# Optimization experiments

Hardware: AMD Instinct MI355X
Metric: run time of the kernel (lower is better)

The kernel has to match this reference:

```python
import jax, jax.numpy as jnp
import numpy as np

EMBED_DIM = 768
HEAD_SIZE = 64

def setup_inputs() -> dict:
    key = jax.random.key(0)
    k1, k2, k3, k4 = jax.random.split(key, 4)
    x = jax.random.normal(k1, (4, 4096, EMBED_DIM), dtype=jnp.float32)
    # nn.Linear(E, H, bias=False) weights, stored as [E, H] for y = x @ W
    scale = 1.0 / np.sqrt(EMBED_DIM)
    Wk = jax.random.uniform(k2, (EMBED_DIM, HEAD_SIZE), jnp.float32, -scale, scale)
    Wq = jax.random.uniform(k3, (EMBED_DIM, HEAD_SIZE), jnp.float32, -scale, scale)
    Wv = jax.random.uniform(k4, (EMBED_DIM, HEAD_SIZE), jnp.float32, -scale, scale)
    return {"x": x, "Wk": Wk, "Wq": Wq, "Wv": Wv}

def reference(x, Wk, Wq, Wv):
    # x: [B, S, E]
    E = x.shape[2]
    K = jnp.einsum("bse,eh->bsh", x, Wk)  # [B, S, H]
    Q = jnp.einsum("bse,eh->bsh", x, Wq)
    V = jnp.einsum("bse,eh->bsh", x, Wv)
    # NOTE: original scales by embedding_dim**0.5, not head_size**0.5
    A = jnp.einsum("bqh,bkh->bqk", Q, K) / jnp.sqrt(jnp.asarray(E, x.dtype))
    A = jax.nn.softmax(A, axis=-1)
    # dropout is inference-mode identity
    return jnp.einsum("bqk,bkh->bqh", A, V)
```

## Files before the change

### kernel.cpp

```cpp
#include <hip/hip_runtime.h>

typedef __attribute__((ext_vector_type(8))) short short8;
typedef __attribute__((ext_vector_type(4))) short short4v;
typedef __attribute__((ext_vector_type(4))) float float4v;

__device__ __forceinline__ short f2bf(float f) {
    union { float f; unsigned u; } v; v.f = f;
    return (short)((v.u + 0x7fffu + ((v.u >> 16) & 1u)) >> 16);
}

__device__ __forceinline__ float fast_exp2(float x) {
#if __has_builtin(__builtin_amdgcn_exp2f)
    return __builtin_amdgcn_exp2f(x);
#else
    return exp2f(x);
#endif
}

__device__ __forceinline__ unsigned cvt_pk_bf16(float lo, float hi) {
    unsigned r;
    asm("v_cvt_pk_bf16_f32 %0, %1, %2" : "=v"(r) : "v"(lo), "v"(hi));
    return r;
}

__global__ void wtrans_kernel(const float* __restrict__ Wk, const float* __restrict__ Wq,
                              const float* __restrict__ Wv, short* __restrict__ Wt3T) {
    int idx = blockIdx.x * 256 + threadIdx.x;
    int p = idx / 12288;
    int rem = idx - p * 12288;
    int kstep = rem / 512;
    int r2 = rem - kstep * 512;
    int lane = r2 >> 3, i = r2 & 7;
    int quad = lane >> 4, l16 = lane & 15;
    int j = p >> 2, nt = p & 3;
    int n = nt * 16 + l16;
    int k = kstep * 32 + quad * 8 + i;
    const float* W = (j == 0) ? Wq : (j == 1 ? Wk : Wv);
    float scale = (j == 0) ? 0.05205877f : 1.0f;
    Wt3T[idx] = f2bf(W[k * 64 + n] * scale);
}

__global__ __launch_bounds__(256, 4) void proj_kernel(
    const float* __restrict__ x, const short* __restrict__ Wt3T,
    short* __restrict__ Qs, short* __restrict__ Kb, short* __restrict__ Vtr)
{
    __shared__ alignas(16) int Abuf[3][256];
    __shared__ alignas(16) short sm[16 * 72];
    const int tid = threadIdx.x;
    const int wave = tid >> 6, lane = tid & 63, quad = lane >> 4, l16 = lane & 15;
    const int m0 = blockIdx.x * 16;
    const int p0 = wave * 3;

    const int xrow = tid >> 4, xcol = (tid & 15) * 2;
    const float* xp = x + (size_t)(m0 + xrow) * 768 + xcol;
    const int aidx = xrow * 16 + (tid & 15);
    const short* wt0 = Wt3T + (size_t)(p0 * 24) * 512 + lane * 8;

    float4v acc[3];
#pragma unroll
    for (int t = 0; t < 3; ++t) acc[t] = (float4v){0.f, 0.f, 0.f, 0.f};

    {
        float2 u = *(const float2*)xp;
        Abuf[0][aidx] = ((unsigned short)f2bf(u.x)) | ((unsigned)f2bf(u.y) << 16);
    }
    short8 Wc0 = *(const short8*)(wt0);
    short8 Wc1 = *(const short8*)(wt0 + 12288);
    short8 Wc2 = *(const short8*)(wt0 + 24576);
    float2 Xn = *(const float2*)(xp + 32);
    __syncthreads();

#pragma unroll
    for (int it = 0; it < 24; ++it) {
        short8 Wn0, Wn1, Wn2;
        float2 Xn2;
        if (it < 23) {
            const short* wn = wt0 + (it + 1) * 512;
            Wn0 = *(const short8*)(wn);
            Wn1 = *(const short8*)(wn + 12288);
            Wn2 = *(const short8*)(wn + 24576);
        }
        if (it < 22) Xn2 = *(const float2*)(xp + (it + 2) * 32);

        short8 a = *(const short8*)((const short*)Abuf[it % 3] + l16 * 32 + quad * 8);
        acc[0] = __builtin_amdgcn_mfma_f32_16x16x32_bf16(a, Wc0, acc[0], 0, 0, 0);
        acc[1] = __builtin_amdgcn_mfma_f32_16x16x32_bf16(a, Wc1, acc[1], 0, 0, 0);
        acc[2] = __builtin_amdgcn_mfma_f32_16x16x32_bf16(a, Wc2, acc[2], 0, 0, 0);

        if (it < 23)
            Abuf[(it + 1) % 3][aidx] = ((unsigned short)f2bf(Xn.x)) | ((unsigned)f2bf(Xn.y) << 16);
        Xn = Xn2;
        Wc0 = Wn0; Wc1 = Wn1; Wc2 = Wn2;
        __syncthreads();
    }

#pragma unroll
    for (int t = 0; t < 3; ++t) {
        const int p = p0 + t, j = p >> 2, nt = p & 3;
        if (j < 2) {
            short* dst = (j == 0) ? Qs : Kb;
#pragma unroll
            for (int r = 0; r < 4; ++r)
                dst[(size_t)(m0 + quad * 4 + r) * 64 + nt * 16 + l16] = f2bf(acc[t][r]);
        } else {
#pragma unroll
            for (int r = 0; r < 4; ++r)
                sm[(quad * 4 + r) * 72 + nt * 16 + l16] = f2bf(acc[t][r]);
        }
    }
    __syncthreads();
    {
        const int h = tid >> 2, si = (tid & 3) * 4;
        const int b = m0 >> 12, s0 = m0 & 4095;
        const int sb = s0 + si;
        const int jb = (sb & ~63) | (sb & 0x23) | ((sb & 0x0C) << 1) | ((sb & 0x10) >> 2);
        short4v tmp;
#pragma unroll
        for (int i = 0; i < 4; ++i) tmp[i] = sm[(si + i) * 72 + h];
        *(short4v*)(Vtr + (size_t)(b * 64 + h) * 4096 + jb) = tmp;
    }
}

__global__ __launch_bounds__(256, 2) void attn_kernel(
    const short* __restrict__ Qs, const short* __restrict__ Kb, const short* __restrict__ Vt,
    float* __restrict__ Opart, float* __restrict__ Ll, int kv_len)
{
    __shared__ alignas(16) short Kl[64 * 72];
    __shared__ alignas(16) short Vl[64 * 72];

    const int tid = threadIdx.x;
    const int wave = tid >> 6, lane = tid & 63, quad = lane >> 4, l16 = lane & 15;
    const int qt = blockIdx.x, b = blockIdx.y, sp = blockIdx.z;
    const int q0 = qt * 128;
    const int bS = b * 4096;
    const int kv0 = sp * kv_len;

    short8 qb[2][2];
#pragma unroll
    for (int ntq = 0; ntq < 2; ++ntq)
#pragma unroll
        for (int ks = 0; ks < 2; ++ks)
            qb[ntq][ks] = *(const short8*)(Qs + (size_t)(bS + q0 + wave * 32 + ntq * 16 + l16) * 64 + ks * 32 + quad * 8);

    float4v o[2][4];
#pragma unroll
    for (int ntq = 0; ntq < 2; ++ntq)
#pragma unroll
        for (int nt = 0; nt < 4; ++nt) o[ntq][nt] = (float4v){0.f, 0.f, 0.f, 0.f};
    float rs[2] = {0.f, 0.f};

    const int sr = tid >> 2, sc = (tid & 3) * 16;

    const short* ksrc0 = Kb + (size_t)(bS + kv0 + sr) * 64 + sc;
    const short* vsrc0 = Vt + (size_t)(b * 64 + sr) * 4096 + kv0 + sc;

    short8 kr0 = *(const short8*)ksrc0;
    short8 kr1 = *(const short8*)(ksrc0 + 8);
    short8 vr0 = *(const short8*)vsrc0;
    short8 vr1 = *(const short8*)(vsrc0 + 8);

    const int ntiles = kv_len >> 6;
    for (int t = 0; t < ntiles; ++t) {
        __syncthreads();
        *(short8*)&Kl[sr * 72 + sc]     = kr0;
        *(short8*)&Kl[sr * 72 + sc + 8] = kr1;
        *(short8*)&Vl[sr * 72 + sc]     = vr0;
        *(short8*)&Vl[sr * 72 + sc + 8] = vr1;
        __syncthreads();

        if (t + 1 < ntiles) {
            const short* kn = ksrc0 + (size_t)(t + 1) * 4096;
            kr0 = *(const short8*)kn;
            kr1 = *(const short8*)(kn + 8);
            const short* vn = vsrc0 + (t + 1) * 64;
            vr0 = *(const short8*)vn;
            vr1 = *(const short8*)(vn + 8);
        }

        union { unsigned u[8]; short8 h[2]; } pa0, pa1;
#pragma unroll
        for (int mtk = 0; mtk < 4; ++mtk) {
            short8 k0 = *(const short8*)&Kl[(mtk * 16 + l16) * 72 + quad * 8];
            short8 k1 = *(const short8*)&Kl[(mtk * 16 + l16) * 72 + 32 + quad * 8];
            float4v s0 = (float4v){0.f, 0.f, 0.f, 0.f};
            float4v s1 = (float4v){0.f, 0.f, 0.f, 0.f};
            __builtin_amdgcn_s_setprio(1);
            s0 = __builtin_amdgcn_mfma_f32_16x16x32_bf16(k0, qb[0][0], s0, 0, 0, 0);
            s0 = __builtin_amdgcn_mfma_f32_16x16x32_bf16(k1, qb[0][1], s0, 0, 0, 0);
            s1 = __builtin_amdgcn_mfma_f32_16x16x32_bf16(k0, qb[1][0], s1, 0, 0, 0);
            s1 = __builtin_amdgcn_mfma_f32_16x16x32_bf16(k1, qb[1][1], s1, 0, 0, 0);
            __builtin_amdgcn_s_setprio(0);

            float p00 = fast_exp2(s0[0]), p01 = fast_exp2(s0[1]);
            float p02 = fast_exp2(s0[2]), p03 = fast_exp2(s0[3]);
            float p10 = fast_exp2(s1[0]), p11 = fast_exp2(s1[1]);
            float p12 = fast_exp2(s1[2]), p13 = fast_exp2(s1[3]);
            rs[0] += (p00 + p01) + (p02 + p03);
            rs[1] += (p10 + p11) + (p12 + p13);
            pa0.u[mtk * 2]     = cvt_pk_bf16(p00, p01);
            pa0.u[mtk * 2 + 1] = cvt_pk_bf16(p02, p03);
            pa1.u[mtk * 2]     = cvt_pk_bf16(p10, p11);
            pa1.u[mtk * 2 + 1] = cvt_pk_bf16(p12, p13);
        }

#pragma unroll
        for (int ks = 0; ks < 2; ++ks) {
            short8 bf[4];
#pragma unroll
            for (int nt = 0; nt < 4; ++nt)
                bf[nt] = *(const short8*)&Vl[(nt * 16 + l16) * 72 + ks * 32 + quad * 8];
            short8 af0 = pa0.h[ks];
            short8 af1 = pa1.h[ks];
            __builtin_amdgcn_s_setprio(1);
#pragma unroll
            for (int nt = 0; nt < 4; ++nt)
                o[0][nt] = __builtin_amdgcn_mfma_f32_16x16x32_bf16(af0, bf[nt], o[0][nt], 0, 0, 0);
#pragma unroll
            for (int nt = 0; nt < 4; ++nt)
                o[1][nt] = __builtin_amdgcn_mfma_f32_16x16x32_bf16(af1, bf[nt], o[1][nt], 0, 0, 0);
            __builtin_amdgcn_s_setprio(0);
        }
    }

#pragma unroll
    for (int ntq = 0; ntq < 2; ++ntq) {
        rs[ntq] += __shfl_xor(rs[ntq], 16);
        rs[ntq] += __shfl_xor(rs[ntq], 32);
    }

#pragma unroll
    for (int ntq = 0; ntq < 2; ++ntq) {
#pragma unroll
        for (int nt = 0; nt < 4; ++nt)
#pragma unroll
            for (int r = 0; r < 4; ++r) {
                int qrow = q0 + wave * 32 + ntq * 16 + quad * 4 + r;
                Opart[((size_t)sp * 16384 + bS + qrow) * 64 + nt * 16 + l16] = o[ntq][nt][r];
            }
        if (quad == 0)
            Ll[(size_t)sp * 16384 + bS + q0 + wave * 32 + ntq * 16 + l16] = rs[ntq];
    }
}

__global__ void combine_kernel(const float* __restrict__ Opart, const float* __restrict__ Ll,
                               float* __restrict__ out, int nsplit) {
    int idx = blockIdx.x * 256 + threadIdx.x;
    int q = idx >> 6;
    float den = 0.f, num = 0.f;
    for (int s = 0; s < nsplit; ++s) {
        den += Ll[s * 16384 + q];
        num += Opart[(size_t)s * 1048576 + idx];
    }
    out[idx] = num / den;
}

extern "C" void kernel_launch(void* const* d_in, const int* in_sizes, int n_in,
                              void* d_out, int out_size, void* d_ws, size_t ws_size,
                              hipStream_t stream) {
    const float* x  = (const float*)d_in[0];
    const float* Wk = (const float*)d_in[1];
    const float* Wq = (const float*)d_in[2];
    const float* Wv = (const float*)d_in[3];
    float* out = (float*)d_out;

    char* w = (char*)d_ws;
    size_t off = 0;
    auto take = [&](size_t bytes) -> void* {
        void* p = w + off;
        off = (off + bytes + 255) & ~(size_t)255;
        return p;
    };
    short* Qs  = (short*)take((size_t)16384 * 64 * 2);
    short* Kb  = (short*)take((size_t)16384 * 64 * 2);
    short* Vt  = (short*)take((size_t)16384 * 64 * 2);
    short* Wt3 = (short*)take((size_t)3 * 64 * 768 * 2);

    size_t base = off;
    int nsplit = 4;
    while (nsplit > 1) {
        size_t need = base + (((size_t)nsplit * 16384 * 4 + 255) & ~(size_t)255)
                      + (size_t)nsplit * 16384 * 64 * 4 + 512;
        if (need <= ws_size) break;
        nsplit >>= 1;
    }
    float* Ll    = (float*)take((size_t)nsplit * 16384 * 4);
    float* Opart = (float*)take((size_t)nsplit * 16384 * 64 * 4);

    wtrans_kernel<<<576, 256, 0, stream>>>(Wk, Wq, Wv, Wt3);
    proj_kernel<<<1024, 256, 0, stream>>>(x, Wt3, Qs, Kb, Vt);
    dim3 ag(32, 4, nsplit);
    attn_kernel<<<ag, 256, 0, stream>>>(Qs, Kb, Vt, Opart, Ll, 4096 / nsplit);
    combine_kernel<<<4096, 256, 0, stream>>>(Opart, Ll, out, nsplit);
}
```

Before: 133.2 us.

## Double-buffer K/V tiles in LDS and double query rows per wave

Each wave now processes 64 query rows instead of 32, so every K/V tile loaded into LDS is reused across twice as many queries and the grid is halved. K/V shared tiles are double-buffered, so the next tile is written to the alternate buffer after compute and only one barrier is needed per iteration. The cost is more registers (launch bounds lowered to 1 block per CU) and fewer blocks in flight, which lowers occupancy and could leave CUs underused.

```diff
diff --git a/kernel.cpp b/kernel.cpp
--- a/kernel.cpp
+++ b/kernel.cpp
@@ -121,124 +121,147 @@
     }
 }
 
-__global__ __launch_bounds__(256, 2) void attn_kernel(
+__global__ __launch_bounds__(256, 1) void attn_kernel(
     const short* __restrict__ Qs, const short* __restrict__ Kb, const short* __restrict__ Vt,
     float* __restrict__ Opart, float* __restrict__ Ll, int kv_len)
 {
-    __shared__ alignas(16) short Kl[64 * 72];
-    __shared__ alignas(16) short Vl[64 * 72];
+    __shared__ alignas(16) short Kl[2][64 * 72];
+    __shared__ alignas(16) short Vl[2][64 * 72];
 
     const int tid = threadIdx.x;
     const int wave = tid >> 6, lane = tid & 63, quad = lane >> 4, l16 = lane & 15;
     const int qt = blockIdx.x, b = blockIdx.y, sp = blockIdx.z;
-    const int q0 = qt * 128;
+    const int q0 = qt * 256;
     const int bS = b * 4096;
     const int kv0 = sp * kv_len;
 
-    short8 qb[2][2];
-#pragma unroll
-    for (int ntq = 0; ntq < 2; ++ntq)
+    short8 qb[4][2];
+#pragma unroll
+    for (int ntq = 0; ntq < 4; ++ntq)
 #pragma unroll
         for (int ks = 0; ks < 2; ++ks)
-            qb[ntq][ks] = *(const short8*)(Qs + (size_t)(bS + q0 + wave * 32 + ntq * 16 + l16) * 64 + ks * 32 + quad * 8);
-
-    float4v o[2][4];
-#pragma unroll
-    for (int ntq = 0; ntq < 2; ++ntq)
+            qb[ntq][ks] = *(const short8*)(Qs + (size_t)(bS + q0 + wave * 64 + ntq * 16 + l16) * 64 + ks * 32 + quad * 8);
+
+    float4v o[4][4];
+#pragma unroll
+    for (int ntq = 0; ntq < 4; ++ntq)
 #pragma unroll
         for (int nt = 0; nt < 4; ++nt) o[ntq][nt] = (float4v){0.f, 0.f, 0.f, 0.f};
-    float rs[2] = {0.f, 0.f};
+    float rs[4] = {0.f, 0.f, 0.f, 0.f};
 
     const int sr = tid >> 2, sc = (tid & 3) * 16;
 
     const short* ksrc0 = Kb + (size_t)(bS + kv0 + sr) * 64 + sc;
     const short* vsrc0 = Vt + (size_t)(b * 64 + sr) * 4096 + kv0 + sc;
+
+    const int ntiles = kv_len >> 6;
 
     short8 kr0 = *(const short8*)ksrc0;
     short8 kr1 = *(const short8*)(ksrc0 + 8);
     short8 vr0 = *(const short8*)vsrc0;
     short8 vr1 = *(const short8*)(vsrc0 + 8);
-
-    const int ntiles = kv_len >> 6;
+    *(short8*)&Kl[0][sr * 72 + sc]     = kr0;
+    *(short8*)&Kl[0][sr * 72 + sc + 8] = kr1;
+    *(short8*)&Vl[0][sr * 72 + sc]     = vr0;
+    *(short8*)&Vl[0][sr * 72 + sc + 8] = vr1;
+    if (ntiles > 1) {
+        const short* kn = ksrc0 + (size_t)4096;
+        kr0 = *(const short8*)kn;
+        kr1 = *(const short8*)(kn + 8);
+        const short* vn = vsrc0 + 64;
+        vr0 = *(const short8*)vn;
+        vr1 = *(const short8*)(vn + 8);
+    }
+    __syncthreads();
+
     for (int t = 0; t < ntiles; ++t) {
-        __syncthreads();
-        *(short8*)&Kl[sr * 72 + sc]     = kr0;
-        *(short8*)&Kl[sr * 72 + sc + 8] = kr1;
-        *(short8*)&Vl[sr * 72 + sc]     = vr0;
-        *(short8*)&Vl[sr * 72 + sc + 8] = vr1;
-        __syncthreads();
+        const int c = t & 1;
+        const short* klc = &Kl[c][0];
+        const short* vlc = &Vl[c][0];
+
+        union { unsigned u[8]; short8 h[2]; } pa0, pa1, pa2, pa3;
+#pragma unroll
+        for (int mtk = 0; mtk < 4; ++mtk) {
+            short8 k0 = *(const short8*)&klc[(mtk * 16 + l16) * 72 + quad * 8];
+            short8 k1 = *(const short8*)&klc[(mtk * 16 + l16) * 72 + 32 + quad * 8];
+#define QK_NTQ(PA, NTQ)                                                          \
+            {                                                                    \
+                float4v s = (float4v){0.f, 0.f, 0.f, 0.f};                       \
+                __builtin_amdgcn_s_setprio(1);                                   \
+                s = __builtin_amdgcn_mfma_f32_16x16x32_bf16(k0, qb[NTQ][0], s, 0, 0, 0); \
+                s = __builtin_amdgcn_mfma_f32_16x16x32_bf16(k1, qb[NTQ][1], s, 0, 0, 0); \
+                __builtin_amdgcn_s_setprio(0);                                   \
+                float e0 = fast_exp2(s[0]), e1 = fast_exp2(s[1]);                \
+                float e2 = fast_exp2(s[2]), e3 = fast_exp2(s[3]);                \
+                rs[NTQ] += (e0 + e1) + (e2 + e3);                                \
+                PA.u[mtk * 2]     = cvt_pk_bf16(e0, e1);                         \
+                PA.u[mtk * 2 + 1] = cvt_pk_bf16(e2, e3);                         \
+            }
+            QK_NTQ(pa0, 0)
+            QK_NTQ(pa1, 1)
+            QK_NTQ(pa2, 2)
+            QK_NTQ(pa3, 3)
+#undef QK_NTQ
+        }
+
+#pragma unroll
+        for (int ks = 0; ks < 2; ++ks) {
+            short8 bf[4];
+#pragma unroll
+            for (int nt = 0; nt < 4; ++nt)
+                bf[nt] = *(const short8*)&vlc[(nt * 16 + l16) * 72 + ks * 32 + quad * 8];
+            __builtin_amdgcn_s_setprio(1);
+#pragma unroll
+            for (int nt = 0; nt < 4; ++nt)
+                o[0][nt] = __builtin_amdgcn_mfma_f32_16x16x32_bf16(pa0.h[ks], bf[nt], o[0][nt], 0, 0, 0);
+#pragma unroll
+            for (int nt = 0; nt < 4; ++nt)
+                o[1][nt] = __builtin_amdgcn_mfma_f32_16x16x32_bf16(pa1.h[ks], bf[nt], o[1][nt], 0, 0, 0);
+#pragma unroll
+            for (int nt = 0; nt < 4; ++nt)
+                o[2][nt] = __builtin_amdgcn_mfma_f32_16x16x32_bf16(pa2.h[ks], bf[nt], o[2][nt], 0, 0, 0);
+#pragma unroll
+            for (int nt = 0; nt < 4; ++nt)
+                o[3][nt] = __builtin_amdgcn_mfma_f32_16x16x32_bf16(pa3.h[ks], bf[nt], o[3][nt], 0, 0, 0);
+            __builtin_amdgcn_s_setprio(0);
+        }
 
         if (t + 1 < ntiles) {
-            const short* kn = ksrc0 + (size_t)(t + 1) * 4096;
+            short* kd = &Kl[c ^ 1][0];
+            short* vd = &Vl[c ^ 1][0];
+            *(short8*)&kd[sr * 72 + sc]     = kr0;
+            *(short8*)&kd[sr * 72 + sc + 8] = kr1;
+            *(short8*)&vd[sr * 72 + sc]     = vr0;
+            *(short8*)&vd[sr * 72 + sc + 8] = vr1;
+        }
+        if (t + 2 < ntiles) {
+            const short* kn = ksrc0 + (size_t)(t + 2) * 4096;
             kr0 = *(const short8*)kn;
             kr1 = *(const short8*)(kn + 8);
-            const short* vn = vsrc0 + (t + 1) * 64;
+            const short* vn = vsrc0 + (t + 2) * 64;
             vr0 = *(const short8*)vn;
             vr1 = *(const short8*)(vn + 8);
         }
-
-        union { unsigned u[8]; short8 h[2]; } pa0, pa1;
-#pragma unroll
-        for (int mtk = 0; mtk < 4; ++mtk) {
-            short8 k0 = *(const short8*)&Kl[(mtk * 16 + l16) * 72 + quad * 8];
-            short8 k1 = *(const short8*)&Kl[(mtk * 16 + l16) * 72 + 32 + quad * 8];
-            float4v s0 = (float4v){0.f, 0.f, 0.f, 0.f};
-            float4v s1 = (float4v){0.f, 0.f, 0.f, 0.f};
-            __builtin_amdgcn_s_setprio(1);
-            s0 = __builtin_amdgcn_mfma_f32_16x16x32_bf16(k0, qb[0][0], s0, 0, 0, 0);
-            s0 = __builtin_amdgcn_mfma_f32_16x16x32_bf16(k1, qb[0][1], s0, 0, 0, 0);
-            s1 = __builtin_amdgcn_mfma_f32_16x16x32_bf16(k0, qb[1][0], s1, 0, 0, 0);
-            s1 = __builtin_amdgcn_mfma_f32_16x16x32_bf16(k1, qb[1][1], s1, 0, 0, 0);
-            __builtin_amdgcn_s_setprio(0);
-
-            float p00 = fast_exp2(s0[0]), p01 = fast_exp2(s0[1]);
-            float p02 = fast_exp2(s0[2]), p03 = fast_exp2(s0[3]);
-            float p10 = fast_exp2(s1[0]), p11 = fast_exp2(s1[1]);
-            float p12 = fast_exp2(s1[2]), p13 = fast_exp2(s1[3]);
-            rs[0] += (p00 + p01) + (p02 + p03);
-            rs[1] += (p10 + p11) + (p12 + p13);
-            pa0.u[mtk * 2]     = cvt_pk_bf16(p00, p01);
-            pa0.u[mtk * 2 + 1] = cvt_pk_bf16(p02, p03);
-            pa1.u[mtk * 2]     = cvt_pk_bf16(p10, p11);
-            pa1.u[mtk * 2 + 1] = cvt_pk_bf16(p12, p13);
-        }
-
-#pragma unroll
-        for (int ks = 0; ks < 2; ++ks) {
-            short8 bf[4];
-#pragma unroll
-            for (int nt = 0; nt < 4; ++nt)
-                bf[nt] = *(const short8*)&Vl[(nt * 16 + l16) * 72 + ks * 32 + quad * 8];
-            short8 af0 = pa0.h[ks];
-            short8 af1 = pa1.h[ks];
-            __builtin_amdgcn_s_setprio(1);
-#pragma unroll
-            for (int nt = 0; nt < 4; ++nt)
-                o[0][nt] = __builtin_amdgcn_mfma_f32_16x16x32_bf16(af0, bf[nt], o[0][nt], 0, 0, 0);
-#pragma unroll
-            for (int nt = 0; nt < 4; ++nt)
-                o[1][nt] = __builtin_amdgcn_mfma_f32_16x16x32_bf16(af1, bf[nt], o[1][nt], 0, 0, 0);
-            __builtin_amdgcn_s_setprio(0);
-        }
-    }
-
-#pragma unroll
-    for (int ntq = 0; ntq < 2; ++ntq) {
+        __syncthreads();
+    }
+
+#pragma unroll
+    for (int ntq = 0; ntq < 4; ++ntq) {
         rs[ntq] += __shfl_xor(rs[ntq], 16);
         rs[ntq] += __shfl_xor(rs[ntq], 32);
     }
 
 #pragma unroll
-    for (int ntq = 0; ntq < 2; ++ntq) {
+    for (int ntq = 0; ntq < 4; ++ntq) {
 #pragma unroll
         for (int nt = 0; nt < 4; ++nt)
 #pragma unroll
             for (int r = 0; r < 4; ++r) {
-                int qrow = q0 + wave * 32 + ntq * 16 + quad * 4 + r;
+                int qrow = q0 + wave * 64 + ntq * 16 + quad * 4 + r;
                 Opart[((size_t)sp * 16384 + bS + qrow) * 64 + nt * 16 + l16] = o[ntq][nt][r];
             }
         if (quad == 0)
-            Ll[(size_t)sp * 16384 + bS + q0 + wave * 32 + ntq * 16 + l16] = rs[ntq];
+            Ll[(size_t)sp * 16384 + bS + q0 + wave * 64 + ntq * 16 + l16] = rs[ntq];
     }
 }
 
@@ -288,7 +311,7 @@
 
     wtrans_kernel<<<576, 256, 0, stream>>>(Wk, Wq, Wv, Wt3);
     proj_kernel<<<1024, 256, 0, stream>>>(x, Wt3, Qs, Kb, Vt);
-    dim3 ag(32, 4, nsplit);
+    dim3 ag(16, 4, nsplit);
     attn_kernel<<<ag, 256, 0, stream>>>(Qs, Kb, Vt, Opart, Ll, 4096 / nsplit);
     combine_kernel<<<4096, 256, 0, stream>>>(Opart, Ll, out, nsplit);
 }
```

Result: slower. 140.0 us (+5.1%).

## Restructure projection kernel to load x directly into MFMA fragments without LDS

Applied to the files above, without the earlier changes.

The QKV projection kernel now has each wave own a 16-row strip and half of the 12 output tiles, loading x straight from global memory in MFMA fragment layout and converting it with packed bf16 conversion instructions. This removes the LDS staging buffer and the per-iteration block barriers, and writes the V transpose directly from registers instead of through shared memory. The cost is that x is read twice per strip (once by each half-wave pair), register pressure is higher with six accumulators and six prefetched weight fragments, and occupancy is lowered to 2 blocks with half as many blocks launched.

```diff
diff --git a/kernel.cpp b/kernel.cpp
--- a/kernel.cpp
+++ b/kernel.cpp
@@ -40,84 +40,74 @@
     Wt3T[idx] = f2bf(W[k * 64 + n] * scale);
 }
 
-__global__ __launch_bounds__(256, 4) void proj_kernel(
+__global__ __launch_bounds__(256, 2) void proj_kernel(
     const float* __restrict__ x, const short* __restrict__ Wt3T,
     short* __restrict__ Qs, short* __restrict__ Kb, short* __restrict__ Vtr)
 {
-    __shared__ alignas(16) int Abuf[3][256];
-    __shared__ alignas(16) short sm[16 * 72];
     const int tid = threadIdx.x;
     const int wave = tid >> 6, lane = tid & 63, quad = lane >> 4, l16 = lane & 15;
-    const int m0 = blockIdx.x * 16;
-    const int p0 = wave * 3;
-
-    const int xrow = tid >> 4, xcol = (tid & 15) * 2;
-    const float* xp = x + (size_t)(m0 + xrow) * 768 + xcol;
-    const int aidx = xrow * 16 + (tid & 15);
-    const short* wt0 = Wt3T + (size_t)(p0 * 24) * 512 + lane * 8;
-
-    float4v acc[3];
-#pragma unroll
-    for (int t = 0; t < 3; ++t) acc[t] = (float4v){0.f, 0.f, 0.f, 0.f};
-
-    {
-        float2 u = *(const float2*)xp;
-        Abuf[0][aidx] = ((unsigned short)f2bf(u.x)) | ((unsigned)f2bf(u.y) << 16);
-    }
-    short8 Wc0 = *(const short8*)(wt0);
-    short8 Wc1 = *(const short8*)(wt0 + 12288);
-    short8 Wc2 = *(const short8*)(wt0 + 24576);
-    float2 Xn = *(const float2*)(xp + 32);
-    __syncthreads();
+    const int strip = blockIdx.x * 32 + (wave >> 1) * 16;
+    const int half = wave & 1;
+
+    const float* xp = x + (size_t)(strip + l16) * 768 + quad * 8;
+    const short* wt0 = Wt3T + (size_t)(half * 6) * 12288 + lane * 8;
+
+    float4v acc[6];
+#pragma unroll
+    for (int t = 0; t < 6; ++t) acc[t] = (float4v){0.f, 0.f, 0.f, 0.f};
+
+    float4 xa = *(const float4*)(xp);
+    float4 xb = *(const float4*)(xp + 4);
+    short8 wf[6];
+#pragma unroll
+    for (int t = 0; t < 6; ++t) wf[t] = *(const short8*)(wt0 + t * 12288);
 
 #pragma unroll
     for (int it = 0; it < 24; ++it) {
-        short8 Wn0, Wn1, Wn2;
-        float2 Xn2;
+        float4 xa2, xb2;
+        short8 wn[6];
         if (it < 23) {
-            const short* wn = wt0 + (it + 1) * 512;
-            Wn0 = *(const short8*)(wn);
-            Wn1 = *(const short8*)(wn + 12288);
-            Wn2 = *(const short8*)(wn + 24576);
-        }
-        if (it < 22) Xn2 = *(const float2*)(xp + (it + 2) * 32);
-
-        short8 a = *(const short8*)((const short*)Abuf[it % 3] + l16 * 32 + quad * 8);
-        acc[0] = __builtin_amdgcn_mfma_f32_16x16x32_bf16(a, Wc0, acc[0], 0, 0, 0);
-        acc[1] = __builtin_amdgcn_mfma_f32_16x16x32_bf16(a, Wc1, acc[1], 0, 0, 0);
-        acc[2] = __builtin_amdgcn_mfma_f32_16x16x32_bf16(a, Wc2, acc[2], 0, 0, 0);
-
-        if (it < 23)
-            Abuf[(it + 1) % 3][aidx] = ((unsigned short)f2bf(Xn.x)) | ((unsigned)f2bf(Xn.y) << 16);
-        Xn = Xn2;
-        Wc0 = Wn0; Wc1 = Wn1; Wc2 = Wn2;
-        __syncthreads();
-    }
-
-#pragma unroll
-    for (int t = 0; t < 3; ++t) {
-        const int p = p0 + t, j = p >> 2, nt = p & 3;
+            const float* xn = xp + (it + 1) * 32;
+            xa2 = *(const float4*)(xn);
+            xb2 = *(const float4*)(xn + 4);
+            const short* wp = wt0 + (it + 1) * 512;
+#pragma unroll
+            for (int t = 0; t < 6; ++t) wn[t] = *(const short8*)(wp + t * 12288);
+        }
+
+        union { unsigned u[4]; short8 h; } af;
+        af.u[0] = cvt_pk_bf16(xa.x, xa.y);
+        af.u[1] = cvt_pk_bf16(xa.z, xa.w);
+        af.u[2] = cvt_pk_bf16(xb.x, xb.y);
+        af.u[3] = cvt_pk_bf16(xb.z, xb.w);
+
+#pragma unroll
+        for (int t = 0; t < 6; ++t)
+            acc[t] = __builtin_amdgcn_mfma_f32_16x16x32_bf16(af.h, wf[t], acc[t], 0, 0, 0);
+
+        xa = xa2; xb = xb2;
+#pragma unroll
+        for (int t = 0; t < 6; ++t) wf[t] = wn[t];
+    }
+
+#pragma unroll
+    for (int t = 0; t < 6; ++t) {
+        const int p = half * 6 + t, j = p >> 2, nt = p & 3;
         if (j < 2) {
             short* dst = (j == 0) ? Qs : Kb;
 #pragma unroll
             for (int r = 0; r < 4; ++r)
-                dst[(size_t)(m0 + quad * 4 + r) * 64 + nt * 16 + l16] = f2bf(acc[t][r]);
+                dst[(size_t)(strip + quad * 4 + r) * 64 + nt * 16 + l16] = f2bf(acc[t][r]);
         } else {
-#pragma unroll
-            for (int r = 0; r < 4; ++r)
-                sm[(quad * 4 + r) * 72 + nt * 16 + l16] = f2bf(acc[t][r]);
-        }
-    }
-    __syncthreads();
-    {
-        const int h = tid >> 2, si = (tid & 3) * 4;
-        const int b = m0 >> 12, s0 = m0 & 4095;
-        const int sb = s0 + si;
-        const int jb = (sb & ~63) | (sb & 0x23) | ((sb & 0x0C) << 1) | ((sb & 0x10) >> 2);
-        short4v tmp;
-#pragma unroll
-        for (int i = 0; i < 4; ++i) tmp[i] = sm[(si + i) * 72 + h];
-        *(short4v*)(Vtr + (size_t)(b * 64 + h) * 4096 + jb) = tmp;
+            const int b = strip >> 12, s0 = strip & 4095;
+            const int h = nt * 16 + l16;
+            const int ks = (s0 >> 5) & 1, hi = (s0 >> 4) & 1;
+            const int jb = (s0 & ~63) | (ks << 5) | (quad << 3) | (hi << 2);
+            short4v tmp;
+#pragma unroll
+            for (int r = 0; r < 4; ++r) tmp[r] = f2bf(acc[t][r]);
+            *(short4v*)(Vtr + (size_t)(b * 64 + h) * 4096 + jb) = tmp;
+        }
     }
 }
 
@@ -287,7 +277,7 @@
     float* Opart = (float*)take((size_t)nsplit * 16384 * 64 * 4);
 
     wtrans_kernel<<<576, 256, 0, stream>>>(Wk, Wq, Wv, Wt3);
-    proj_kernel<<<1024, 256, 0, stream>>>(x, Wt3, Qs, Kb, Vt);
+    proj_kernel<<<512, 256, 0, stream>>>(x, Wt3, Qs, Kb, Vt);
     dim3 ag(32, 4, nsplit);
     attn_kernel<<<ag, 256, 0, stream>>>(Qs, Kb, Vt, Opart, Ll, 4096 / nsplit);
     combine_kernel<<<4096, 256, 0, stream>>>(Opart, Ll, out, nsplit);
```

Measured after the change: 141.7 us. +6.4%, slower.
